# Optimization experiments

Measured on AMD Instinct MI355X. Metric: run time of the kernel, lower is better.

The kernel has to match this reference:

```python
import jax, jax.numpy as jnp
import numpy as np


def setup_inputs() -> dict:
    key = jax.random.key(0)
    k1, k2, k3 = jax.random.split(key, 3)
    B, N, C, H, W = 16, 100, 256, 100, 152
    OH, OW = 800, 1216
    feature_map = jax.random.normal(k1, (B, C, H, W), dtype=jnp.float32)
    u = jax.random.uniform(k2, (B, N, 4), dtype=jnp.float32)
    # boxes in original-image coords: x,y top-left, w,h sizes (>= a few pixels)
    x = u[..., 0] * (OW * 0.7)
    y = u[..., 1] * (OH * 0.7)
    w = u[..., 2] * (OW * 0.3) + 8.0
    h = u[..., 3] * (OH * 0.3) + 8.0
    keypoints = jnp.stack([x, y, w, h], axis=-1)
    mask = jax.random.randint(k3, (B, N), 0, 2).astype(jnp.int32)
    return {"feature_map": feature_map, "keypoints": keypoints, "mask": mask,
            "original_H": OH, "original_W": OW}


def _roi_mean_pool(feature_map, keypoints, mask, original_H, original_W):
    B, C, H, W = feature_map.shape
    sx = W / original_W
    sy = H / original_H
    x, y, w, h = keypoints[..., 0], keypoints[..., 1], keypoints[..., 2], keypoints[..., 3]
    # int() in torch truncates toward zero; coords here are non-negative
    xr = jnp.clip((x * sx).astype(jnp.int32), 0, W - 1)          # [B,N]
    yr = jnp.clip((y * sy).astype(jnp.int32), 0, H - 1)
    wr = jnp.minimum(jnp.maximum((w * sx).astype(jnp.int32), 1), W - xr)
    hr = jnp.minimum(jnp.maximum((h * sy).astype(jnp.int32), 1), H - yr)
    # integral image trick: adaptive_avg_pool2d to (1,1) == mean over the ROI window
    S = jnp.cumsum(jnp.cumsum(feature_map, axis=2), axis=3)
    S = jnp.pad(S, ((0, 0), (0, 0), (1, 0), (1, 0)))             # [B,C,H+1,W+1]
    y0, y1 = yr, yr + hr
    x0, x1 = xr, xr + wr

    def take(Sb, yy, xx):  # Sb: [C,H+1,W+1]; yy,xx: [N] -> [C,N]
        return Sb[:, yy, xx]

    g = jax.vmap(take)
    sums = g(S, y1, x1) - g(S, y0, x1) - g(S, y1, x0) + g(S, y0, x0)  # [B,C,N]
    area = (hr * wr).astype(feature_map.dtype)                        # [B,N]
    mean = jnp.transpose(sums, (0, 2, 1)) / area[:, :, None]          # [B,N,C]
    return jnp.where(mask[:, :, None] > 0, mean, jnp.zeros((), feature_map.dtype))


def reference(feature_map, keypoints, mask, original_H, original_W):
    return _roi_mean_pool(feature_map, keypoints, mask, original_H, original_W)
```

## Files before the change

### kernel.cpp

```cpp
#include <hip/hip_runtime.h>

#define THREADS 128
#define MAXOFF 1536
#define CSPLIT 8
#define CPG 16

__global__ __launch_bounds__(THREADS) void roi_pool_kernel(
    const float* __restrict__ fmap,
    const float* __restrict__ kps,
    const int*   __restrict__ maskp,
    const int*   __restrict__ pOH,
    const int*   __restrict__ pOW,
    float*       __restrict__ out,
    int B, int N, int C, int H, int W)
{
    __shared__ int offs[MAXOFF];

    const int blk  = blockIdx.x;
    const int bn   = blk / CSPLIT;
    const int csec = blk - bn * CSPLIT;
    const int b    = bn / N;
    const int HW   = H * W;
    const int Csec = C / CSPLIT;

    const float sx = (float)W / (float)(*pOW);
    const float sy = (float)H / (float)(*pOH);

    const float* kp = kps + (size_t)bn * 4;
    const float x = kp[0], y = kp[1], w = kp[2], h = kp[3];
    int xr = (int)(x * sx); xr = min(max(xr, 0), W - 1);
    int yr = (int)(y * sy); yr = min(max(yr, 0), H - 1);
    int wr = (int)(w * sx); wr = min(max(wr, 1), W - xr);
    int hr = (int)(h * sy); hr = min(max(hr, 1), H - yr);

    float* outp = out + (size_t)bn * C + csec * Csec;
    if (maskp[bn] <= 0) {
        for (int c = threadIdx.x; c < Csec; c += THREADS) outp[c] = 0.0f;
        return;
    }

    const int   area     = hr * wr;
    const float inv_area = 1.0f / (float)area;
    const float* fb = fmap + (size_t)b * C * HW + (size_t)(csec * Csec) * HW
                    + (size_t)yr * W + xr;

    for (int idx = threadIdx.x; idx < area; idx += THREADS) {
        const int yy = idx / wr;
        offs[idx] = yy * W + (idx - yy * wr);
    }
    __syncthreads();

    const int lane  = threadIdx.x & 63;
    const int wave  = threadIdx.x >> 6;
    const int kfull = area >> 6;
    const int cg    = wave * CPG;

    const float* fc = fb + (size_t)cg * HW;
    float acc[CPG];
    #pragma unroll
    for (int u = 0; u < CPG; ++u) acc[u] = 0.0f;

    for (int k = 0; k < kfull; ++k) {
        const int off = offs[(k << 6) + lane];
        #pragma unroll
        for (int u = 0; u < CPG; ++u)
            acc[u] += fc[(size_t)u * HW + off];
    }
    const int j = (kfull << 6) + lane;
    if (j < area) {
        const int off = offs[j];
        #pragma unroll
        for (int u = 0; u < CPG; ++u)
            acc[u] += fc[(size_t)u * HW + off];
    }

    float outv = 0.0f;
    #pragma unroll
    for (int u = 0; u < CPG; ++u) {
        float v = acc[u];
        #pragma unroll
        for (int o = 32; o > 0; o >>= 1) v += __shfl_xor(v, o);
        if (lane == u) outv = v * inv_area;
    }
    if (lane < CPG) outp[cg + lane] = outv;
}

extern "C" void kernel_launch(void* const* d_in, const int* in_sizes, int n_in,
                              void* d_out, int out_size, void* d_ws, size_t ws_size,
                              hipStream_t stream) {
    const float* fmap  = (const float*)d_in[0];
    const float* kps   = (const float*)d_in[1];
    const int*   maskp = (const int*)d_in[2];
    const int*   pOH   = (const int*)d_in[3];
    const int*   pOW   = (const int*)d_in[4];
    float* out = (float*)d_out;

    const int N  = 100;
    const int BN = in_sizes[2];
    const int B  = BN / N;
    const int C  = out_size / BN;
    const int H  = 100, W = 152;

    roi_pool_kernel<<<dim3(BN * CSPLIT), dim3(THREADS), 0, stream>>>(
        fmap, kps, maskp, pOH, pOW, out, B, N, C, H, W);
}
```

Measured before the change: 72.09 us.

## Replace shared-memory offset table with masked float4 vectorized ROI loads

Drops the shared-memory offset table and its __syncthreads, and instead has each lane load aligned float4 chunks covering the ROI row span. Lanes derive their row and column by float reciprocal division and zero out columns outside the window with per-component masks. This cuts the number of load instructions and removes the index setup phase. In exchange it reads some wasted edge elements, and the float division used for the row index could be inexact for large cell counts.

```diff
diff --git a/kernel.cpp b/kernel.cpp
--- a/kernel.cpp
+++ b/kernel.cpp
@@ -1,7 +1,6 @@
 #include <hip/hip_runtime.h>
 
 #define THREADS 128
-#define MAXOFF 1536
 #define CSPLIT 8
 #define CPG 16
 
@@ -14,8 +13,6 @@
     float*       __restrict__ out,
     int B, int N, int C, int H, int W)
 {
-    __shared__ int offs[MAXOFF];
-
     const int blk  = blockIdx.x;
     const int bn   = blk / CSPLIT;
     const int csec = blk - bn * CSPLIT;
@@ -41,37 +38,43 @@
 
     const int   area     = hr * wr;
     const float inv_area = 1.0f / (float)area;
-    const float* fb = fmap + (size_t)b * C * HW + (size_t)(csec * Csec) * HW
-                    + (size_t)yr * W + xr;
+    const float* fb = fmap + (size_t)b * C * HW + (size_t)(csec * Csec) * HW;
 
-    for (int idx = threadIdx.x; idx < area; idx += THREADS) {
-        const int yy = idx / wr;
-        offs[idx] = yy * W + (idx - yy * wr);
-    }
-    __syncthreads();
+    const int q0    = xr >> 2;
+    const int q1    = (xr + wr - 1) >> 2;
+    const int wq    = q1 - q0 + 1;
+    const int ncell = hr * wq;
+    const int x1    = xr + wr;
 
-    const int lane  = threadIdx.x & 63;
-    const int wave  = threadIdx.x >> 6;
-    const int kfull = area >> 6;
-    const int cg    = wave * CPG;
+    const int lane = threadIdx.x & 63;
+    const int wave = threadIdx.x >> 6;
+    const int cg   = wave * CPG;
 
     const float* fc = fb + (size_t)cg * HW;
     float acc[CPG];
     #pragma unroll
     for (int u = 0; u < CPG; ++u) acc[u] = 0.0f;
 
-    for (int k = 0; k < kfull; ++k) {
-        const int off = offs[(k << 6) + lane];
+    const int   kmax   = (ncell + 63) >> 6;
+    const float inv_wq = 1.0f / (float)wq;
+    for (int k = 0; k < kmax; ++k) {
+        const int   j     = (k << 6) + lane;
+        const int   jj    = min(j, ncell - 1);
+        const int   yy    = (int)(((float)jj + 0.5f) * inv_wq);
+        const int   col   = jj - yy * wq;
+        const int   colx  = (q0 + col) << 2;
+        const int   off   = (yr + yy) * W + colx;
+        const float valid = (j < ncell) ? 1.0f : 0.0f;
+        float4 m;
+        m.x = (colx     >= xr && colx     < x1) ? valid : 0.0f;
+        m.y = (colx + 1 >= xr && colx + 1 < x1) ? valid : 0.0f;
+        m.z = (colx + 2 >= xr && colx + 2 < x1) ? valid : 0.0f;
+        m.w = (colx + 3 >= xr && colx + 3 < x1) ? valid : 0.0f;
         #pragma unroll
-        for (int u = 0; u < CPG; ++u)
-            acc[u] += fc[(size_t)u * HW + off];
-    }
-    const int j = (kfull << 6) + lane;
-    if (j < area) {
-        const int off = offs[j];
-        #pragma unroll
-        for (int u = 0; u < CPG; ++u)
-            acc[u] += fc[(size_t)u * HW + off];
+        for (int u = 0; u < CPG; ++u) {
+            const float4 v = *(const float4*)(fc + (size_t)u * HW + off);
+            acc[u] += v.x * m.x + v.y * m.y + v.z * m.z + v.w * m.w;
+        }
     }
 
     float outv = 0.0f;
```

Measured after the change: 69.34 us. 1.04x faster.
